# Performance work log

Measured on AMD Instinct MI355X. Metric: run time of the kernel, lower is better.

Reference implementation:

```python
import jax, jax.numpy as jnp
import numpy as np

D_MODEL = 1024
HEADS = 16
DK = D_MODEL // HEADS  # 64
B, S = 1, 4096


def setup_inputs() -> dict:
    key = jax.random.key(0)
    ks = jax.random.split(key, 11)
    sd = 1.0 / np.sqrt(D_MODEL)
    return {
        "q": jax.random.normal(ks[0], (B, S, D_MODEL), jnp.float32),
        "k": jax.random.normal(ks[1], (B, S, D_MODEL), jnp.float32),
        "v": jax.random.normal(ks[2], (B, S, D_MODEL), jnp.float32),
        "Wq": jax.random.uniform(ks[3], (D_MODEL, D_MODEL), jnp.float32, -sd, sd),
        "bq": jax.random.uniform(ks[4], (D_MODEL,), jnp.float32, -sd, sd),
        "Wk": jax.random.uniform(ks[5], (D_MODEL, DK), jnp.float32, -sd, sd),
        "bk": jax.random.uniform(ks[6], (DK,), jnp.float32, -sd, sd),
        "Wv": jax.random.uniform(ks[7], (D_MODEL, DK), jnp.float32, -sd, sd),
        "bv": jax.random.uniform(ks[8], (DK,), jnp.float32, -sd, sd),
        "Wo": jax.random.uniform(ks[9], (D_MODEL, D_MODEL), jnp.float32, -sd, sd),
        "bo": jax.random.uniform(ks[10], (D_MODEL,), jnp.float32, -sd, sd),
    }


def reference(q, k, v, Wq, bq, Wk, bk, Wv, bv, Wo, bo):
    b, s, d = q.shape
    # projections: q -> [b, H, s, dk]; k, v -> single shared head [b, s, dk]
    qp = (q @ Wq + bq).reshape(b, s, HEADS, DK).transpose(0, 2, 1, 3)
    kp = k @ Wk + bk  # [b, s, dk]
    vp = v @ Wv + bv  # [b, s, dk]
    # NOTE: original module never applies self.scale or dropout — faithful.
    scores = jnp.einsum('bhqd,bkd->bhqk', qp, kp)  # [b, H, s, s]
    attn = jax.nn.softmax(scores, axis=-1)
    out = jnp.einsum('bhqk,bkd->bhqd', attn, vp)  # [b, H, s, dk]
    out = out.transpose(0, 2, 1, 3).reshape(b, s, d)
    return out @ Wo + bo
```

## Files before the change

### kernel.cpp

```cpp
#include <hip/hip_runtime.h>
#include <hip/hip_bf16.h>
#include <stdint.h>

typedef __bf16 bf16_t;
typedef __attribute__((ext_vector_type(8))) __bf16 bf16x8;
typedef __attribute__((ext_vector_type(4))) __bf16 bf16x4;
typedef __attribute__((ext_vector_type(4))) float f32x4;

#define S_LEN 4096
#define DMODEL 1024
#define NHEADS 16
#define DKH 64

#if defined(__has_builtin)
#if __has_builtin(__builtin_amdgcn_exp2f)
#define EXP2F(x) __builtin_amdgcn_exp2f(x)
#endif
#endif
#ifndef EXP2F
#define EXP2F(x) __expf((x)*0.6931471805599453f)
#endif

__device__ __forceinline__ f32x4 mfma16(bf16x8 a, bf16x8 b, f32x4 c) {
  return __builtin_amdgcn_mfma_f32_16x16x32_bf16(a, b, c, 0, 0, 0);
}

template <typename TS>
__device__ __forceinline__ bf16x8 load8_bf16(const TS* g) {
  bf16x8 o;
  if constexpr (sizeof(TS) == 4) {
    const float4 f0 = *(const float4*)(g);
    const float4 f1 = *(const float4*)(g + 4);
    o[0] = (bf16_t)f0.x; o[1] = (bf16_t)f0.y; o[2] = (bf16_t)f0.z; o[3] = (bf16_t)f0.w;
    o[4] = (bf16_t)f1.x; o[5] = (bf16_t)f1.y; o[6] = (bf16_t)f1.z; o[7] = (bf16_t)f1.w;
  } else {
    o = *(const bf16x8*)(g);
  }
  return o;
}

template <typename TS>
__device__ __forceinline__ void stage_tile64(const TS* __restrict__ g, int gstride,
                                             bf16_t* lds, int rows, int tid) {
  for (int i = tid; i < rows * 8; i += 256) {
    const int row = i >> 3, j = i & 7;
    const int c = j ^ (row & 7);
    bf16x8 v = load8_bf16(g + (size_t)row * gstride + j * 8);
    *(bf16x8*)((char*)lds + row * 128 + c * 16) = v;
  }
}

__device__ __forceinline__ bf16x8 frag64(const bf16_t* lds, int row, int g) {
  return *(const bf16x8*)((const char*)lds + row * 128 + ((g ^ (row & 7)) * 16));
}

__device__ __forceinline__ void gload16(const bf16_t* g, bf16_t* lds) {
  __builtin_amdgcn_global_load_lds(
      (const __attribute__((address_space(1))) unsigned int*)g,
      (__attribute__((address_space(3))) unsigned int*)lds, 16, 0, 0);
}

__global__ __launch_bounds__(256) void convert_bf16(const float* __restrict__ src,
                                                    bf16_t* __restrict__ dst) {
  const size_t i = (size_t)(blockIdx.x * 256 + threadIdx.x) * 8;
  bf16x8 v = load8_bf16(src + i);
  *(bf16x8*)(dst + i) = v;
}

__global__ __launch_bounds__(256) void prep_weights(const float* __restrict__ Wq,
                                                    const float* __restrict__ Wo,
                                                    const float* __restrict__ Wk,
                                                    const float* __restrict__ Wv,
                                                    const float* __restrict__ qsrc,
                                                    bf16_t* __restrict__ Wqt,
                                                    bf16_t* __restrict__ Wot,
                                                    bf16_t* __restrict__ Wkt,
                                                    bf16_t* __restrict__ Wvt,
                                                    bf16_t* __restrict__ qdst) {
  const int b = blockIdx.x;
  const int tid = threadIdx.x;
  if (b >= 544) {
    const size_t i = ((size_t)(b - 544) * 256 + tid) * 8;
    bf16x8 v = load8_bf16(qsrc + i);
    *(bf16x8*)(qdst + i) = v;
    return;
  }
  const float* src; bf16_t* dst; int ss, ds_, bx, by;
  if (b < 256)      { src = Wq; dst = Wqt; ss = 1024; ds_ = 1024; bx = b & 15;         by = b >> 4; }
  else if (b < 512) { src = Wo; dst = Wot; ss = 1024; ds_ = 1024; bx = (b - 256) & 15; by = (b - 256) >> 4; }
  else if (b < 528) { src = Wk; dst = Wkt; ss = 64;   ds_ = 1024; bx = 0;              by = b - 512; }
  else              { src = Wv; dst = Wvt; ss = 64;   ds_ = 1024; bx = 0;              by = b - 528; }

  __shared__ bf16_t t[64][65];
  const int r0 = by * 64, c0 = bx * 64;
#pragma unroll
  for (int it = 0; it < 2; ++it) {
    int idx = tid + it * 256;
    int r = idx >> 3, c8 = idx & 7;
    bf16x8 v = load8_bf16(src + (size_t)(r0 + r) * ss + c0 + c8 * 8);
#pragma unroll
    for (int j = 0; j < 8; ++j) t[c8 * 8 + j][r] = v[j];
  }
  __syncthreads();
#pragma unroll
  for (int it = 0; it < 2; ++it) {
    int idx = tid + it * 256;
    int r = idx >> 3, c8 = idx & 7;
    bf16x8 v;
#pragma unroll
    for (int j = 0; j < 8; ++j) v[j] = t[r][c8 * 8 + j];
    *(bf16x8*)(dst + (size_t)(c0 + r) * ds_ + r0 + c8 * 8) = v;
  }
}

template <typename TC>
__device__ __forceinline__ void gemm_body_dma(char* smem,
                                              const bf16_t* __restrict__ A, int lda,
                                              const bf16_t* __restrict__ Bt, int ldb,
                                              const float* __restrict__ bias,
                                              TC* __restrict__ C, int ldc, int K,
                                              float escale, int m0, int n0) {
  constexpr int BM = 128, BN = 64;
  bf16_t* As = (bf16_t*)smem;
  bf16_t* Bs = (bf16_t*)(smem + 32768);
  const int tid = threadIdx.x, l = tid & 63, w = tid >> 6;
  const int lr = l & 15, quad = l >> 4;
  const int wm = w * 32;

  const int srow = l >> 3;
  const int sch = (l & 7) ^ srow;
  const bf16_t* a0 = A + (size_t)(m0 + w * 32 + srow) * lda + sch * 8;
  const bf16_t* b0 = Bt + (size_t)(n0 + w * 16 + srow) * ldb + sch * 8;

  f32x4 zero = {0.f, 0.f, 0.f, 0.f};
  f32x4 acc[2][4];
#pragma unroll
  for (int i = 0; i < 2; ++i)
#pragma unroll
    for (int j = 0; j < 4; ++j) acc[i][j] = zero;

  const int nt = K >> 6;

#pragma unroll
  for (int sub = 0; sub < 4; ++sub)
    gload16(a0 + (size_t)sub * 8 * lda, &As[(w * 32 + sub * 8) * 64]);
#pragma unroll
  for (int sub = 0; sub < 2; ++sub)
    gload16(b0 + (size_t)sub * 8 * ldb, &Bs[(w * 16 + sub * 8) * 64]);
  asm volatile("s_waitcnt vmcnt(0)" ::: "memory");
  __builtin_amdgcn_s_barrier();
  asm volatile("" ::: "memory");

  for (int t = 0; t < nt; ++t) {
    const int cur = t & 1;
    if (t + 1 < nt) {
#pragma unroll
      for (int sub = 0; sub < 4; ++sub)
        gload16(a0 + (size_t)(t + 1) * 64 + (size_t)sub * 8 * lda,
                &As[(cur ^ 1) * BM * 64 + (w * 32 + sub * 8) * 64]);
#pragma unroll
      for (int sub = 0; sub < 2; ++sub)
        gload16(b0 + (size_t)(t + 1) * 64 + (size_t)sub * 8 * ldb,
                &Bs[(cur ^ 1) * BN * 64 + (w * 16 + sub * 8) * 64]);
    }
    const bf16_t* Ac = &As[cur * BM * 64];
    const bf16_t* Bc = &Bs[cur * BN * 64];
#pragma unroll
    for (int kc = 0; kc < 2; ++kc) {
      bf16x8 af[2], bfr[4];
#pragma unroll
      for (int rt = 0; rt < 2; ++rt) af[rt] = frag64(Ac, wm + rt * 16 + lr, kc * 4 + quad);
#pragma unroll
      for (int ct = 0; ct < 4; ++ct) bfr[ct] = frag64(Bc, ct * 16 + lr, kc * 4 + quad);
#pragma unroll
      for (int rt = 0; rt < 2; ++rt)
#pragma unroll
        for (int ct = 0; ct < 4; ++ct) acc[rt][ct] = mfma16(af[rt], bfr[ct], acc[rt][ct]);
    }
    asm volatile("s_waitcnt vmcnt(0) lgkmcnt(0)" ::: "memory");
    __builtin_amdgcn_s_barrier();
    asm volatile("" ::: "memory");
  }

#pragma unroll
  for (int rt = 0; rt < 2; ++rt)
#pragma unroll
    for (int ct = 0; ct < 4; ++ct) {
      const int n = n0 + ct * 16 + lr;
      const float bv = bias[n];
      const int mb = m0 + wm + rt * 16 + quad * 4;
#pragma unroll
      for (int r = 0; r < 4; ++r)
        C[(size_t)(mb + r) * ldc + n] = (TC)((acc[rt][ct][r] + bv) * escale);
    }
}

template <typename TC>
__global__ __launch_bounds__(256) void gemm_nt_dma(const bf16_t* __restrict__ A, int lda,
                                                   const bf16_t* __restrict__ Bt, int ldb,
                                                   const float* __restrict__ bias,
                                                   TC* __restrict__ C, int ldc, int K,
                                                   float escale) {
  __shared__ __align__(16) char smem[49152];
  gemm_body_dma<TC>(smem, A, lda, Bt, ldb, bias, C, ldc, K, escale,
                    blockIdx.y * 128, blockIdx.x * 64);
}

template <int KSPLIT>
__device__ __forceinline__ void projkv_body(char* smem,
                                            const float* __restrict__ A,
                                            const bf16_t* __restrict__ Bt,
                                            float* __restrict__ part,
                                            int kp, int m0) {
  bf16_t* As = (bf16_t*)smem;
  bf16_t* Bs = (bf16_t*)(smem + 16384);
  const int tid = threadIdx.x, l = tid & 63, w = tid >> 6;
  const int lr = l & 15, quad = l >> 4;
  const int kBase = kp * (DMODEL / KSPLIT);
  const int wm = w * 32;

  f32x4 zero = {0.f, 0.f, 0.f, 0.f};
  f32x4 acc[2][4];
#pragma unroll
  for (int i = 0; i < 2; ++i)
#pragma unroll
    for (int j = 0; j < 4; ++j) acc[i][j] = zero;

  for (int t = 0; t < (DMODEL / KSPLIT) / 64; ++t) {
    __syncthreads();
    stage_tile64(A + (size_t)m0 * DMODEL + kBase + t * 64, DMODEL, As, 128, tid);
    stage_tile64(Bt + kBase + t * 64, DMODEL, Bs, 64, tid);
    __syncthreads();
#pragma unroll
    for (int kc = 0; kc < 2; ++kc) {
      bf16x8 af[2], bfr[4];
#pragma unroll
      for (int rt = 0; rt < 2; ++rt) af[rt] = frag64(As, wm + rt * 16 + lr, kc * 4 + quad);
#pragma unroll
      for (int ct = 0; ct < 4; ++ct) bfr[ct] = frag64(Bs, ct * 16 + lr, kc * 4 + quad);
#pragma unroll
      for (int rt = 0; rt < 2; ++rt)
#pragma unroll
        for (int ct = 0; ct < 4; ++ct) acc[rt][ct] = mfma16(af[rt], bfr[ct], acc[rt][ct]);
    }
  }
#pragma unroll
  for (int rt = 0; rt < 2; ++rt)
#pragma unroll
    for (int ct = 0; ct < 4; ++ct) {
      const int n = ct * 16 + lr;
      const int mb = m0 + wm + rt * 16 + quad * 4;
#pragma unroll
      for (int r = 0; r < 4; ++r)
        part[(size_t)kp * S_LEN * 64 + (size_t)(mb + r) * 64 + n] = acc[rt][ct][r];
    }
}

template <int KSPLIT>
__global__ __launch_bounds__(256) void gemm_projkv_partial(const float* __restrict__ Ak,
                                                           const float* __restrict__ Av,
                                                           const bf16_t* __restrict__ Wkt,
                                                           const bf16_t* __restrict__ Wvt,
                                                           float* __restrict__ Pk,
                                                           float* __restrict__ Pv) {
  __shared__ __align__(16) char smem[24576];
  projkv_body<KSPLIT>(smem, blockIdx.z ? Av : Ak, blockIdx.z ? Wvt : Wkt,
                      blockIdx.z ? Pv : Pk, blockIdx.x, blockIdx.y * 128);
}

__global__ __launch_bounds__(256) void mid_gemms(const bf16_t* __restrict__ qb,
                                                 const bf16_t* __restrict__ Wqt,
                                                 const float* __restrict__ bq,
                                                 bf16_t* __restrict__ qp,
                                                 const float* __restrict__ k,
                                                 const float* __restrict__ v,
                                                 const bf16_t* __restrict__ Wkt,
                                                 const bf16_t* __restrict__ Wvt,
                                                 float* __restrict__ Pk,
                                                 float* __restrict__ Pv,
                                                 float escale) {
  __shared__ __align__(16) char smem[49152];
  const int flat = blockIdx.x;
  if (flat < 512) {
    gemm_body_dma<bf16_t>(smem, qb, 1024, Wqt, 1024, bq, qp, 1024, 1024, escale,
                          (flat >> 4) * 128, (flat & 15) * 64);
  } else {
    const int j = flat - 512;
    const int z = j >> 7;
    const int jj = j & 127;
    projkv_body<4>(smem, z ? v : k, z ? Wvt : Wkt, z ? Pv : Pk, jj & 3, (jj >> 2) * 128);
  }
}

template <int KSPLIT>
__global__ __launch_bounds__(512) void reduce_kv(const float* __restrict__ Pk,
                                                 const float* __restrict__ Pv,
                                                 const float* __restrict__ bk,
                                                 const float* __restrict__ bv,
                                                 bf16_t* __restrict__ kvb,
                                                 bf16_t* __restrict__ vtb) {
  __shared__ bf16_t t[32][65];
  const int tid = threadIdx.x;
  const int s0 = blockIdx.x * 32;
  const int d = tid & 63;
  const int sgrp = tid >> 6;
  const float bkd = bk[d], bvd = bv[d];
#pragma unroll
  for (int i = 0; i < 4; ++i) {
    const int s_local = sgrp * 4 + i;
    const int gid = (s0 + s_local) * 64 + d;
    float sk = bkd, sv = bvd;
#pragma unroll
    for (int p = 0; p < KSPLIT; ++p) {
      sk += Pk[(size_t)p * S_LEN * 64 + gid];
      sv += Pv[(size_t)p * S_LEN * 64 + gid];
    }
    kvb[(size_t)(s0 + s_local) * 128 + d] = (bf16_t)sk;
    kvb[(size_t)(s0 + s_local) * 128 + 64 + d] = (bf16_t)sv;
    t[s_local][d] = (bf16_t)sv;
  }
  __syncthreads();
  if (tid < 256) {
    const int dl = tid >> 2;
    const int s8 = tid & 3;
    bf16x8 v;
#pragma unroll
    for (int j = 0; j < 8; ++j) v[j] = t[s8 * 8 + j][dl];
    *(bf16x8*)(vtb + (size_t)dl * S_LEN + s0 + s8 * 8) = v;
  }
}

__global__ __launch_bounds__(512, 4) void mqa_attn(const bf16_t* __restrict__ qp,
                                                   const bf16_t* __restrict__ kvb,
                                                   const bf16_t* __restrict__ vtb,
                                                   bf16_t* __restrict__ outp) {
  __shared__ __align__(16) char smem[49152];
  bf16_t* Ks = (bf16_t*)smem;
  bf16_t* Vs = (bf16_t*)(smem + 16384);
  char*   Ps = smem + 32768;

  const int tid = threadIdx.x, l = tid & 63, w = tid >> 6;
  const int lr = l & 15, quad = l >> 4;
  const int wq = w >> 1, wk = w & 1;
  const int h = blockIdx.y;
  const int q0 = blockIdx.x * 128;
  const int qrA = q0 + wq * 32 + lr;
  const int qrB = qrA + 16;
  char* Pw = Ps + w * 2048;

  const int srow = w * 8 + (l >> 3);
  const int schunk = (l & 7) ^ (srow & 7);
  const bf16_t* ksrc = kvb + (size_t)srow * 128 + schunk * 8;
  const bf16_t* vsrc = vtb + (size_t)srow * S_LEN + schunk * 8;

  const bf16_t* qbA = qp + (size_t)qrA * DMODEL + h * DKH;
  const bf16x8 qfA0 = *(const bf16x8*)(qbA + quad * 8);
  const bf16x8 qfA1 = *(const bf16x8*)(qbA + 32 + quad * 8);
  const bf16_t* qbB = qp + (size_t)qrB * DMODEL + h * DKH;
  const bf16x8 qfB0 = *(const bf16x8*)(qbB + quad * 8);
  const bf16x8 qfB1 = *(const bf16x8*)(qbB + 32 + quad * 8);

  f32x4 zero = {0.f, 0.f, 0.f, 0.f};
  f32x4 o[4][2];
#pragma unroll
  for (int dt = 0; dt < 4; ++dt) { o[dt][0] = zero; o[dt][1] = zero; }
  float liA = 0.f, liB = 0.f;

  gload16(ksrc, Ks + w * 512);
  gload16(vsrc, Vs + w * 512);
  asm volatile("s_waitcnt vmcnt(0)" ::: "memory");
  __builtin_amdgcn_s_barrier();
  asm volatile("" ::: "memory");

  for (int t = 0; t < S_LEN / 64; ++t) {
    const int cur = t & 1;
    if (t + 1 < S_LEN / 64) {
      gload16(ksrc + (size_t)(t + 1) * 8192, Ks + (cur ^ 1) * 4096 + w * 512);
      gload16(vsrc + (size_t)(t + 1) * 64, Vs + (cur ^ 1) * 4096 + w * 512);
    }
    const bf16_t* Kc = Ks + cur * 4096;
    const bf16_t* Vc = Vs + cur * 4096;

    f32x4 st[2][2];
#pragma unroll
    for (int kt = 0; kt < 2; ++kt) {
      const int krow = wk * 32 + kt * 16 + lr;
      const bf16x8 kf0 = frag64(Kc, krow, quad);
      const bf16x8 kf1 = frag64(Kc, krow, 4 + quad);
      f32x4 a0 = mfma16(kf0, qfA0, zero);
      a0 = mfma16(kf1, qfA1, a0);
      st[kt][0] = a0;
      f32x4 a1 = mfma16(kf0, qfB0, zero);
      a1 = mfma16(kf1, qfB1, a1);
      st[kt][1] = a1;
    }

#pragma unroll
    for (int kt = 0; kt < 2; ++kt)
#pragma unroll
      for (int qt = 0; qt < 2; ++qt) {
        bf16x4 pk;
        float rs = 0.f;
#pragma unroll
        for (int r = 0; r < 4; ++r) {
          const float p = EXP2F(st[kt][qt][r]);
          rs += p;
          pk[r] = (bf16_t)p;
        }
        if (qt == 0) liA += rs; else liB += rs;
        *(bf16x4*)(Pw + lr * 128 +
                   ((((qt << 2) + (kt << 1) + (quad >> 1)) ^ (lr & 7)) << 4) +
                   ((quad & 1) << 3)) = pk;
      }
    asm volatile("s_waitcnt lgkmcnt(0)" ::: "memory");

    const bf16x8 pf0 = *(const bf16x8*)(Pw + lr * 128 + ((quad ^ (lr & 7)) << 4));
    const bf16x8 pf1 = *(const bf16x8*)(Pw + lr * 128 + (((4 + quad) ^ (lr & 7)) << 4));
#pragma unroll
    for (int dt = 0; dt < 4; ++dt) {
      const bf16x8 vf = frag64(Vc, dt * 16 + lr, wk * 4 + quad);
      o[dt][0] = mfma16(vf, pf0, o[dt][0]);
      o[dt][1] = mfma16(vf, pf1, o[dt][1]);
    }

    asm volatile("s_waitcnt vmcnt(0) lgkmcnt(0)" ::: "memory");
    __builtin_amdgcn_s_barrier();
    asm volatile("" ::: "memory");
  }

  liA += __shfl_xor(liA, 16, 64);
  liA += __shfl_xor(liA, 32, 64);
  liB += __shfl_xor(liB, 16, 64);
  liB += __shfl_xor(liB, 32, 64);

  float* liBuf = (float*)Ps;
  if (quad == 0) {
    liBuf[w * 32 + lr] = liA;
    liBuf[w * 32 + 16 + lr] = liB;
  }
  float* Obuf = (float*)smem;
  if (wk == 1) {
#pragma unroll
    for (int dt = 0; dt < 4; ++dt)
#pragma unroll
      for (int qt = 0; qt < 2; ++qt)
        *(f32x4*)(&Obuf[wq * 2048 + (qt * 16 + lr) * 64 + dt * 16 + quad * 4]) = o[dt][qt];
  }
  __syncthreads();
  if (wk == 0) {
    const float ltA = liA + liBuf[(w ^ 1) * 32 + lr];
    const float ltB = liB + liBuf[(w ^ 1) * 32 + 16 + lr];
    const float invA = 1.f / ltA;
    const float invB = 1.f / ltB;
#pragma unroll
    for (int dt = 0; dt < 4; ++dt) {
      const f32x4 pA = *(const f32x4*)(&Obuf[wq * 2048 + lr * 64 + dt * 16 + quad * 4]);
      const f32x4 pB = *(const f32x4*)(&Obuf[wq * 2048 + (16 + lr) * 64 + dt * 16 + quad * 4]);
      bf16x4 ovA, ovB;
#pragma unroll
      for (int rg = 0; rg < 4; ++rg) {
        ovA[rg] = (bf16_t)((o[dt][0][rg] + pA[rg]) * invA);
        ovB[rg] = (bf16_t)((o[dt][1][rg] + pB[rg]) * invB);
      }
      *(bf16x4*)(outp + (size_t)qrA * DMODEL + h * DKH + dt * 16 + quad * 4) = ovA;
      *(bf16x4*)(outp + (size_t)qrB * DMODEL + h * DKH + dt * 16 + quad * 4) = ovB;
    }
  }
}

extern "C" void kernel_launch(void* const* d_in, const int* in_sizes, int n_in,
                              void* d_out, int out_size, void* d_ws, size_t ws_size,
                              hipStream_t stream) {
  const float* q  = (const float*)d_in[0];
  const float* k  = (const float*)d_in[1];
  const float* v  = (const float*)d_in[2];
  const float* Wq = (const float*)d_in[3];
  const float* bq = (const float*)d_in[4];
  const float* Wk = (const float*)d_in[5];
  const float* bk = (const float*)d_in[6];
  const float* Wv = (const float*)d_in[7];
  const float* bv = (const float*)d_in[8];
  const float* Wo = (const float*)d_in[9];
  const float* bo = (const float*)d_in[10];
  float* out = (float*)d_out;
  char* ws = (char*)d_ws;

  const size_t MB = 1u << 20;
  bf16_t* Wqt = (bf16_t*)(ws);
  bf16_t* Wot = (bf16_t*)(ws + 2 * MB);
  bf16_t* Wkt = (bf16_t*)(ws + 4 * MB);
  bf16_t* Wvt = (bf16_t*)(ws + 4 * MB + 131072);
  bf16_t* kvb = (bf16_t*)(ws + 4 * MB + 524288);
  bf16_t* vtb = (bf16_t*)(ws + 5 * MB + 524288);

  const bool bigws = ws_size >= (size_t)30 * MB;
  dim3 B(256);
  const float LOG2E = 1.44269504088896340736f;

  if (bigws) {
    float*  Pk   = (float*)(ws + 6 * MB);
    float*  Pv   = (float*)(ws + 10 * MB);
    bf16_t* qp   = (bf16_t*)(ws + 14 * MB);
    bf16_t* qb   = (bf16_t*)(ws + 22 * MB);
    bf16_t* attn = (bf16_t*)(ws + 6 * MB);

    prep_weights<<<dim3(2592), B, 0, stream>>>(Wq, Wo, Wk, Wv, q, Wqt, Wot, Wkt, Wvt, qb);
    mid_gemms<<<dim3(768), B, 0, stream>>>(qb, Wqt, bq, qp, k, v, Wkt, Wvt, Pk, Pv, LOG2E);
    reduce_kv<4><<<dim3(128), dim3(512), 0, stream>>>(Pk, Pv, bk, bv, kvb, vtb);
    mqa_attn<<<dim3(32, 16), dim3(512), 0, stream>>>(qp, kvb, vtb, attn);
    gemm_nt_dma<float><<<dim3(16, 32), B, 0, stream>>>(attn, 1024, Wot, 1024, bo, out,
                                                       1024, 1024, 1.0f);
  } else {
    float*  Pk   = (float*)(ws + 6 * MB);
    float*  Pv   = (float*)(ws + 14 * MB);
    bf16_t* qp   = (bf16_t*)(ws + 14 * MB);
    bf16_t* qb   = (bf16_t*)(ws + 6 * MB);
    bf16_t* attn = (bf16_t*)(ws + 6 * MB);

    prep_weights<<<dim3(544), B, 0, stream>>>(Wq, Wo, Wk, Wv, q, Wqt, Wot, Wkt, Wvt, qb);
    gemm_projkv_partial<8><<<dim3(8, 32, 2), B, 0, stream>>>(k, v, Wkt, Wvt, Pk, Pv);
    reduce_kv<8><<<dim3(128), dim3(512), 0, stream>>>(Pk, Pv, bk, bv, kvb, vtb);
    convert_bf16<<<dim3(2048), B, 0, stream>>>(q, qb);
    gemm_nt_dma<bf16_t><<<dim3(16, 32), B, 0, stream>>>(qb, 1024, Wqt, 1024, bq, qp,
                                                        1024, 1024, LOG2E);
    mqa_attn<<<dim3(32, 16), dim3(512), 0, stream>>>(qp, kvb, vtb, attn);
    gemm_nt_dma<float><<<dim3(16, 32), B, 0, stream>>>(attn, 1024, Wot, 1024, bo, out,
                                                       1024, 1024, 1.0f);
  }
}
```

Before: 230.3 us.

## Compute K/V projections directly in mid_gemms and drop split-K reduce kernel

Replaces the split-K K/V projection (partials to fp32 workspace plus a separate reduce_kv launch) with a direct full-K 64-row tile GEMM inside mid_gemms. It adds bias, writes bf16 K/V, and writes V transposed through shared memory. This removes one kernel launch and the fp32 partial-sum round trip through global memory. In exchange there are fewer, longer K/V blocks (128 blocks each looping over all of K), which may become a tail if they are scheduled late next to the Q GEMM blocks; they are placed first in the grid to reduce that risk.

```diff
diff --git a/kernel.cpp b/kernel.cpp
--- a/kernel.cpp
+++ b/kernel.cpp
@@ -268,6 +268,68 @@
                       blockIdx.z ? Pv : Pk, blockIdx.x, blockIdx.y * 128);
 }
 
+__device__ __forceinline__ void projkv_direct64(char* smem,
+                                                const float* __restrict__ A,
+                                                const bf16_t* __restrict__ Bt,
+                                                const float* __restrict__ bias,
+                                                bf16_t* __restrict__ kvb, int koff,
+                                                bf16_t* __restrict__ vtb,
+                                                int m0) {
+  bf16_t* As = (bf16_t*)smem;
+  bf16_t* Bs = (bf16_t*)(smem + 8192);
+  const int tid = threadIdx.x, l = tid & 63, w = tid >> 6;
+  const int lr = l & 15, quad = l >> 4;
+  const int wm = w * 16;
+
+  f32x4 zero = {0.f, 0.f, 0.f, 0.f};
+  f32x4 acc[4];
+#pragma unroll
+  for (int j = 0; j < 4; ++j) acc[j] = zero;
+
+  for (int t = 0; t < 16; ++t) {
+    __syncthreads();
+    stage_tile64(A + (size_t)m0 * DMODEL + t * 64, DMODEL, As, 64, tid);
+    stage_tile64(Bt + t * 64, DMODEL, Bs, 64, tid);
+    __syncthreads();
+#pragma unroll
+    for (int kc = 0; kc < 2; ++kc) {
+      const bf16x8 af = frag64(As, wm + lr, kc * 4 + quad);
+      bf16x8 bfr[4];
+#pragma unroll
+      for (int ct = 0; ct < 4; ++ct) bfr[ct] = frag64(Bs, ct * 16 + lr, kc * 4 + quad);
+#pragma unroll
+      for (int ct = 0; ct < 4; ++ct) acc[ct] = mfma16(af, bfr[ct], acc[ct]);
+    }
+  }
+  __syncthreads();
+  bf16_t* tbuf = (bf16_t*)smem;
+#pragma unroll
+  for (int ct = 0; ct < 4; ++ct) {
+    const int n = ct * 16 + lr;
+    const float bv = bias[n];
+    const int sl = wm + quad * 4;
+#pragma unroll
+    for (int r = 0; r < 4; ++r) {
+      const bf16_t bval = (bf16_t)(acc[ct][r] + bv);
+      kvb[(size_t)(m0 + sl + r) * 128 + koff + n] = bval;
+      if (vtb) tbuf[(sl + r) * 68 + n] = bval;
+    }
+  }
+  if (vtb) {
+    __syncthreads();
+    const int dl = tid >> 2;
+    const int s8 = tid & 3;
+#pragma unroll
+    for (int c = 0; c < 2; ++c) {
+      const int chunk = c * 4 + s8;
+      bf16x8 vv;
+#pragma unroll
+      for (int j = 0; j < 8; ++j) vv[j] = tbuf[(chunk * 8 + j) * 68 + dl];
+      *(bf16x8*)(vtb + (size_t)dl * S_LEN + m0 + chunk * 8) = vv;
+    }
+  }
+}
+
 __global__ __launch_bounds__(256) void mid_gemms(const bf16_t* __restrict__ qb,
                                                  const bf16_t* __restrict__ Wqt,
                                                  const float* __restrict__ bq,
@@ -276,19 +338,22 @@
                                                  const float* __restrict__ v,
                                                  const bf16_t* __restrict__ Wkt,
                                                  const bf16_t* __restrict__ Wvt,
-                                                 float* __restrict__ Pk,
-                                                 float* __restrict__ Pv,
+                                                 const float* __restrict__ bk,
+                                                 const float* __restrict__ bv,
+                                                 bf16_t* __restrict__ kvb,
+                                                 bf16_t* __restrict__ vtb,
                                                  float escale) {
   __shared__ __align__(16) char smem[49152];
   const int flat = blockIdx.x;
-  if (flat < 512) {
+  if (flat < 128) {
+    const int z = flat >> 6;
+    const int m0 = (flat & 63) * 64;
+    projkv_direct64(smem, z ? v : k, z ? Wvt : Wkt, z ? bv : bk,
+                    kvb, z ? 64 : 0, z ? vtb : nullptr, m0);
+  } else {
+    const int j = flat - 128;
     gemm_body_dma<bf16_t>(smem, qb, 1024, Wqt, 1024, bq, qp, 1024, 1024, escale,
-                          (flat >> 4) * 128, (flat & 15) * 64);
-  } else {
-    const int j = flat - 512;
-    const int z = j >> 7;
-    const int jj = j & 127;
-    projkv_body<4>(smem, z ? v : k, z ? Wvt : Wkt, z ? Pv : Pk, jj & 3, (jj >> 2) * 128);
+                          (j >> 4) * 128, (j & 15) * 64);
   }
 }
 
@@ -498,15 +563,13 @@
   const float LOG2E = 1.44269504088896340736f;
 
   if (bigws) {
-    float*  Pk   = (float*)(ws + 6 * MB);
-    float*  Pv   = (float*)(ws + 10 * MB);
     bf16_t* qp   = (bf16_t*)(ws + 14 * MB);
     bf16_t* qb   = (bf16_t*)(ws + 22 * MB);
     bf16_t* attn = (bf16_t*)(ws + 6 * MB);
 
     prep_weights<<<dim3(2592), B, 0, stream>>>(Wq, Wo, Wk, Wv, q, Wqt, Wot, Wkt, Wvt, qb);
-    mid_gemms<<<dim3(768), B, 0, stream>>>(qb, Wqt, bq, qp, k, v, Wkt, Wvt, Pk, Pv, LOG2E);
-    reduce_kv<4><<<dim3(128), dim3(512), 0, stream>>>(Pk, Pv, bk, bv, kvb, vtb);
+    mid_gemms<<<dim3(640), B, 0, stream>>>(qb, Wqt, bq, qp, k, v, Wkt, Wvt, bk, bv,
+                                           kvb, vtb, LOG2E);
     mqa_attn<<<dim3(32, 16), dim3(512), 0, stream>>>(qp, kvb, vtb, attn);
     gemm_nt_dma<float><<<dim3(16, 32), B, 0, stream>>>(attn, 1024, Wot, 1024, bo, out,
                                                        1024, 1024, 1.0f);
```

Result: slower. 239.1 us (+3.9%).
